# Kernel tuning notes

Measured on AMD Instinct MI355X. Metric: run time of the kernel, lower is better.

Reference implementation:

```python
import jax, jax.numpy as jnp
import numpy as np

N = 100000
E = 1600000
G = 256
D_IN = 128
NEURON = 64
ATT_F = 8
K = 3
ALPHA = 0.1


def setup_inputs() -> dict:
    key = jax.random.key(0)
    ks = jax.random.split(key, 12)
    x = jax.random.normal(ks[0], (N, D_IN), dtype=jnp.float32)
    closeness_feature = jax.random.normal(ks[1], (N, ATT_F), dtype=jnp.float32)
    edge_index = jax.random.randint(ks[2], (2, E), 0, N, dtype=jnp.int32)
    batch = jnp.sort(jax.random.randint(ks[3], (N,), 0, G, dtype=jnp.int32))
    s = 0.05
    return {
        "x": x,
        "closeness_feature": closeness_feature,
        "edge_index": edge_index,
        "batch": batch,
        "num_graphs": G,
        "nn1_w": jax.random.normal(ks[4], (D_IN, NEURON), dtype=jnp.float32) * s,
        "nn1_b": jnp.zeros((NEURON,), dtype=jnp.float32),
        "close_w": jax.random.normal(ks[5], (ATT_F, 1), dtype=jnp.float32) * s,
        "close_b": jnp.zeros((1,), dtype=jnp.float32),
        "att1_w": jax.random.normal(ks[6], (NEURON, 16), dtype=jnp.float32) * s,
        "att1_b": jnp.zeros((16,), dtype=jnp.float32),
        "att2_w": jax.random.normal(ks[7], (16, 1), dtype=jnp.float32) * s,
        "att2_b": jnp.zeros((1,), dtype=jnp.float32),
    }


def _appnp(x, edge_index, n):
    # gcn_norm with self-loops: A_hat = D^{-1/2}(A+I)D^{-1/2}
    loop = jnp.arange(n, dtype=edge_index.dtype)
    src = jnp.concatenate([edge_index[0], loop])
    dst = jnp.concatenate([edge_index[1], loop])
    deg = jax.ops.segment_sum(jnp.ones_like(dst, dtype=x.dtype), dst, num_segments=n)
    dinv = jax.lax.rsqrt(deg)  # deg >= 1 due to self loops
    norm = (dinv[src] * dinv[dst])[:, None]  # [E+N, 1]
    h = x
    for _ in range(K):
        agg = jax.ops.segment_sum(norm * h[src], dst, num_segments=n)
        h = (1.0 - ALPHA) * agg + ALPHA * x
    return h


def reference(x, closeness_feature, edge_index, batch, num_graphs,
              nn1_w, nn1_b, close_w, close_b, att1_w, att1_b, att2_w, att2_b):
    n = x.shape[0]
    h = _appnp(x, edge_index, n)                      # [N, D_IN]
    h = jax.nn.relu(h @ nn1_w + nn1_b)                # [N, 64]

    # per-graph softmax over closeness scores (segment softmax)
    logits = (closeness_feature @ close_w + close_b)[:, 0]          # [N]
    m = jax.ops.segment_max(logits, batch, num_segments=num_graphs)  # [G]
    w = jnp.exp(logits - m[batch])
    z = jax.ops.segment_sum(w, batch, num_segments=num_graphs)       # [G]
    p = w / z[batch]                                                 # softmax per graph

    cnt = jax.ops.segment_sum(jnp.ones((n,), dtype=h.dtype), batch,
                              num_segments=num_graphs)               # nodes per graph
    p = p * cnt[batch]                                               # scaled by curr_size

    # self_max: per-graph max over weighted node features
    pooled = jax.ops.segment_max(p[:, None] * h, batch, num_segments=num_graphs)  # [G, 64]

    a = jax.nn.relu(pooled @ att1_w + att1_b)         # [G, 16]
    return a @ att2_w + att2_b                        # [G, 1]
```

## Files before the change

### kernel.cpp

```cpp
#include <hip/hip_runtime.h>
#include <cstdint>
#include <cstddef>


#define DIN 128
#define NEU 64
#define BK2 512
#define BKSHIFT2 9
#define BKCAP 16384
#define ESCAP 12288
#define MAXNB 256
#define ASTAGE 6400

typedef __attribute__((ext_vector_type(8))) short short8v;
typedef __attribute__((ext_vector_type(4))) float f32x4;

__device__ inline float bf2f(unsigned short h) {
    return __uint_as_float(((unsigned)h) << 16);
}
__device__ inline unsigned short f2bf(float f) {
    unsigned u = __float_as_uint(f);
    unsigned r = u + 0x7FFFu + ((u >> 16) & 1u);
    return (unsigned short)(r >> 16);
}


__global__ __launch_bounds__(256) void binA_kernel(
        const int* __restrict__ src, const int* __restrict__ dst,
        int* __restrict__ bcur, int* __restrict__ pk, int E, int NB) {
    __shared__ int hist[MAXNB];
    __shared__ int lstart[MAXNB];
    __shared__ int lcur[MAXNB];
    __shared__ int resv[MAXNB];
    __shared__ int sh[256];
    __shared__ int stage[ASTAGE];
    __shared__ int gidx[ASTAGE];
    int nchunk = gridDim.x;
    int chunk = (E + nchunk - 1) / nchunk;
    int lo = blockIdx.x * chunk;
    int hi = min(E, lo + chunk);
    int t = threadIdx.x;
    for (int b = t; b < NB; b += 256) hist[b] = 0;
    __syncthreads();
    for (int i = lo + t; i < hi; i += 256)
        atomicAdd(&hist[dst[i] >> BKSHIFT2], 1);
    __syncthreads();
    int c = (t < NB) ? hist[t] : 0;
    sh[t] = c;
    __syncthreads();
    for (int d = 1; d < 256; d <<= 1) {
        int u = (t >= d) ? sh[t - d] : 0;
        __syncthreads();
        sh[t] += u;
        __syncthreads();
    }
    if (t < NB) {
        int excl = sh[t] - c;
        lstart[t] = excl;
        lcur[t] = excl;
        resv[t] = atomicAdd(&bcur[t], c);
    }
    __syncthreads();
    for (int i = lo + t; i < hi; i += 256) {
        int d = dst[i], b = d >> BKSHIFT2;
        int p = atomicAdd(&lcur[b], 1);
        stage[p] = (src[i] << BKSHIFT2) | (d & (BK2 - 1));
        gidx[p] = resv[b] + (p - lstart[b]) + b * BKCAP;
    }
    __syncthreads();
    int total = hi - lo;
    for (int q = t; q < total; q += 256)
        pk[gidx[q]] = stage[q];
}


__global__ __launch_bounds__(256) void binB_kernel(
        const int* __restrict__ bcur, const int* __restrict__ pk,
        int* __restrict__ es, int* __restrict__ rowptr,
        float* __restrict__ dinv, int N, int NB) {
    __shared__ int cur[BK2];
    __shared__ int sh[256];
    __shared__ int esl[ESCAP];
    __shared__ int sbase[2];
    int b = blockIdx.x;
    int t = threadIdx.x;
    int node0 = b << BKSHIFT2;
    int v = (t < NB) ? bcur[t] : 0;
    sh[t] = v;
    __syncthreads();
    for (int d = 1; d < 256; d <<= 1) {
        int u = (t >= d) ? sh[t - d] : 0;
        __syncthreads();
        sh[t] += u;
        __syncthreads();
    }
    if (t == b) { sbase[0] = sh[t] - v; sbase[1] = v; }
    __syncthreads();
    int base = sbase[0];
    int count = sbase[1];
    const int* pb = pk + (size_t)b * BKCAP;

    for (int q = t; q < BK2; q += 256) cur[q] = 0;
    __syncthreads();
    for (int i = t; i < count; i += 256)
        atomicAdd(&cur[pb[i] & (BK2 - 1)], 1);
    __syncthreads();
    int c0 = cur[2 * t], c1 = cur[2 * t + 1];
    int s = c0 + c1;
    __syncthreads();
    sh[t] = s;
    __syncthreads();
    for (int d = 1; d < 256; d <<= 1) {
        int u = (t >= d) ? sh[t - d] : 0;
        __syncthreads();
        sh[t] += u;
        __syncthreads();
    }
    int excl = sh[t] - s;
    int n0 = node0 + 2 * t;
    if (n0 < N) {
        rowptr[n0 + 1] = base + excl + c0;
        dinv[n0] = rsqrtf((float)c0 + 1.0f);
    }
    if (n0 + 1 < N) {
        rowptr[n0 + 2] = base + excl + c0 + c1;
        dinv[n0 + 1] = rsqrtf((float)c1 + 1.0f);
    }
    if (b == 0 && t == 0) rowptr[0] = 0;
    __syncthreads();
    cur[2 * t] = excl;
    cur[2 * t + 1] = excl + c0;
    __syncthreads();
    for (int i = t; i < count; i += 256) {
        int w = pb[i];
        int pos = atomicAdd(&cur[w & (BK2 - 1)], 1);
        if (pos < ESCAP) esl[pos] = w >> BKSHIFT2;
    }
    __syncthreads();
    for (int i = t; i < count; i += 256) es[base + i] = esl[i];
}


__global__ __launch_bounds__(256) void fc1_kernel(
        const float* __restrict__ x, const float* __restrict__ W,
        const float* __restrict__ dinv, ushort* __restrict__ yb,
        ushort* __restrict__ g0, ushort* __restrict__ g1,
        ushort* __restrict__ g2, int N) {
    int tid = threadIdx.x;
    if (blockIdx.x == 0 && tid < 48) {
        int buf = tid >> 4, e = tid & 15;
        ushort* gp = (buf == 0) ? g0 : (buf == 1) ? g1 : g2;
        ((ushort4*)(gp + (size_t)N * NEU))[e] = make_ushort4(0, 0, 0, 0);
    }
    __shared__ ushort sW[DIN * NEU];
    for (int k = tid; k < DIN * NEU / 2; k += 256) {
        float2 v = ((const float2*)W)[k];
        ushort2 o;
        o.x = f2bf(v.x);
        o.y = f2bf(v.y);
        ((ushort2*)sW)[k] = o;
    }
    __syncthreads();
    int lane = tid & 63;
    int wv = tid >> 6;
    int l15 = lane & 15;
    int lg = lane >> 4;
    short8v bfrag[4][4];
#pragma unroll
    for (int kt = 0; kt < 4; kt++)
#pragma unroll
        for (int ct = 0; ct < 4; ct++) {
            short8v f;
#pragma unroll
            for (int e = 0; e < 8; e++)
                f[e] = (short)sW[(kt * 32 + lg * 8 + e) * NEU + ct * 16 + l15];
            bfrag[kt][ct] = f;
        }
    long long row0 = (long long)blockIdx.x * 64 + wv * 16;
    if (row0 >= N) return;
    bool rowok = (row0 + l15) < N;
    const float* xr = x + (size_t)(row0 + l15) * DIN;
    f32x4 acc[4];
#pragma unroll
    for (int ct = 0; ct < 4; ct++) acc[ct] = (f32x4){0.f, 0.f, 0.f, 0.f};
#pragma unroll
    for (int kt = 0; kt < 4; kt++) {
        short8v af = (short8v){0, 0, 0, 0, 0, 0, 0, 0};
        if (rowok) {
            float4 v0 = *((const float4*)(xr + kt * 32 + lg * 8));
            float4 v1 = *((const float4*)(xr + kt * 32 + lg * 8 + 4));
            af[0] = (short)f2bf(v0.x); af[1] = (short)f2bf(v0.y);
            af[2] = (short)f2bf(v0.z); af[3] = (short)f2bf(v0.w);
            af[4] = (short)f2bf(v1.x); af[5] = (short)f2bf(v1.y);
            af[6] = (short)f2bf(v1.z); af[7] = (short)f2bf(v1.w);
        }
#pragma unroll
        for (int ct = 0; ct < 4; ct++)
            acc[ct] = __builtin_amdgcn_mfma_f32_16x16x32_bf16(af, bfrag[kt][ct], acc[ct], 0, 0, 0);
    }
#pragma unroll
    for (int r = 0; r < 4; r++) {
        long long rr = row0 + lg * 4 + r;
        if (rr < N) {
            float dv = dinv[rr];
#pragma unroll
            for (int ct = 0; ct < 4; ct++) {
                float v = acc[ct][r];
                yb[(size_t)rr * NEU + ct * 16 + l15] = f2bf(v);
                g0[(size_t)rr * NEU + ct * 16 + l15] = f2bf(dv * v);
            }
        }
    }
}


__device__ inline void acc4(float4& a, ushort4 w) {
    a.x += bf2f(w.x); a.y += bf2f(w.y); a.z += bf2f(w.z); a.w += bf2f(w.w);
}

template <int MODE>
__global__ __launch_bounds__(256) void pull_kernel(
        const int* __restrict__ rowptr, const int* __restrict__ es,
        const float* __restrict__ dinv, const ushort* __restrict__ gin,
        const ushort* __restrict__ yb, const float* __restrict__ b1,
        ushort* __restrict__ gout, float* __restrict__ h2out, int N) {
    int wid = threadIdx.x >> 6;
    int lane = threadIdx.x & 63;
    int quarter = lane >> 4;
    int l16 = lane & 15;
    int node = blockIdx.x * 4 + wid;
    if (node >= N) return;
    int beg = rowptr[node], end = rowptr[node + 1];
    float dd = dinv[node];
    const ushort4* gin4 = (const ushort4*)gin;
    float4 a0 = make_float4(0.f, 0.f, 0.f, 0.f);
    float4 a1 = make_float4(0.f, 0.f, 0.f, 0.f);
    float4 a2 = make_float4(0.f, 0.f, 0.f, 0.f);
    float4 a3 = make_float4(0.f, 0.f, 0.f, 0.f);
    int deg = end - beg;
    for (int base = 0; base < deg; base += 64) {
        int myi = base + lane;
        int msrc = (myi < deg) ? es[beg + myi] : N;
        int cnt = min(64, deg - base);
        int quads = (cnt + 3) >> 2;
        int j = 0;
        for (; j + 3 < quads; j += 4) {
            int s0 = __shfl(msrc, 4 * j + quarter);
            int s1 = __shfl(msrc, 4 * j + 4 + quarter);
            int s2 = __shfl(msrc, 4 * j + 8 + quarter);
            int s3 = __shfl(msrc, 4 * j + 12 + quarter);
            ushort4 w0 = gin4[(uint)(s0 << 4) + l16];
            ushort4 w1 = gin4[(uint)(s1 << 4) + l16];
            ushort4 w2 = gin4[(uint)(s2 << 4) + l16];
            ushort4 w3 = gin4[(uint)(s3 << 4) + l16];
            acc4(a0, w0); acc4(a1, w1); acc4(a2, w2); acc4(a3, w3);
        }
        for (; j < quads; j++) {
            int s0 = __shfl(msrc, 4 * j + quarter);
            ushort4 w0 = gin4[(uint)(s0 << 4) + l16];
            acc4(a0, w0);
        }
    }
    float4 acc;
    acc.x = (a0.x + a1.x) + (a2.x + a3.x);
    acc.y = (a0.y + a1.y) + (a2.y + a3.y);
    acc.z = (a0.z + a1.z) + (a2.z + a3.z);
    acc.w = (a0.w + a1.w) + (a2.w + a3.w);
    acc.x += __shfl_xor(acc.x, 16);
    acc.y += __shfl_xor(acc.y, 16);
    acc.z += __shfl_xor(acc.z, 16);
    acc.w += __shfl_xor(acc.w, 16);
    acc.x += __shfl_xor(acc.x, 32);
    acc.y += __shfl_xor(acc.y, 32);
    acc.z += __shfl_xor(acc.z, 32);
    acc.w += __shfl_xor(acc.w, 32);
    if (quarter == 0) {
        ushort4 gv = *((const ushort4*)(gin + (size_t)node * NEU) + l16);
        ushort4 yv = *((const ushort4*)(yb + (size_t)node * NEU) + l16);
        float c9 = 0.9f * dd;
        float hx = c9 * (acc.x + bf2f(gv.x)) + 0.1f * bf2f(yv.x);
        float hy = c9 * (acc.y + bf2f(gv.y)) + 0.1f * bf2f(yv.y);
        float hz = c9 * (acc.z + bf2f(gv.z)) + 0.1f * bf2f(yv.z);
        float hw = c9 * (acc.w + bf2f(gv.w)) + 0.1f * bf2f(yv.w);
        if (MODE == 1) {
            float4 bb = *((const float4*)b1 + l16);
            float4 o;
            o.x = fmaxf(hx + bb.x, 0.f);
            o.y = fmaxf(hy + bb.y, 0.f);
            o.z = fmaxf(hz + bb.z, 0.f);
            o.w = fmaxf(hw + bb.w, 0.f);
            *((float4*)(h2out + (size_t)node * NEU) + l16) = o;
        } else {
            ushort4 o;
            o.x = f2bf(dd * hx); o.y = f2bf(dd * hy);
            o.z = f2bf(dd * hz); o.w = f2bf(dd * hw);
            *((ushort4*)(gout + (size_t)node * NEU) + l16) = o;
        }
    }
}


__global__ __launch_bounds__(256) void head_kernel(
        const int* __restrict__ batch, const float* __restrict__ cf,
        const float* __restrict__ cw, const float* __restrict__ cb,
        const float* __restrict__ h2, const float* __restrict__ aw1,
        const float* __restrict__ ab1, const float* __restrict__ aw2,
        const float* __restrict__ ab2, float* __restrict__ out, int N) {
    int g = blockIdx.x;
    int tid = threadIdx.x;
    __shared__ int sbound[2];
    __shared__ float redm[256];
    __shared__ float redz[256];
    __shared__ float pooled[64];
    __shared__ float sa[16];
    if (tid < 2) {
        int target = g + tid;
        int lo = 0, hi = N;
        while (lo < hi) {
            int mid = (lo + hi) >> 1;
            if (batch[mid] < target) lo = mid + 1; else hi = mid;
        }
        sbound[tid] = lo;
    }
    __syncthreads();
    int s0 = sbound[0], e0 = sbound[1];
    float w0 = cw[0], w1 = cw[1], w2 = cw[2], w3 = cw[3];
    float w4 = cw[4], w5 = cw[5], w6 = cw[6], w7 = cw[7];
    float cb0 = cb[0];
    float m = -INFINITY, z = 0.f;
    for (int i = s0 + tid; i < e0; i += 256) {
        const float4* c = (const float4*)(cf + (size_t)i * 8);
        float4 A = c[0], B = c[1];
        float l = A.x * w0 + A.y * w1 + A.z * w2 + A.w * w3
                + B.x * w4 + B.y * w5 + B.z * w6 + B.w * w7 + cb0;
        float mn = fmaxf(m, l);
        z = z * __expf(m - mn) + __expf(l - mn);
        m = mn;
    }
    redm[tid] = m; redz[tid] = z;
    __syncthreads();
    for (int w = 128; w > 0; w >>= 1) {
        if (tid < w) {
            float ma = redm[tid], mb = redm[tid + w];
            float za = redz[tid], zb = redz[tid + w];
            float mn = fmaxf(ma, mb);
            redz[tid] = (mn == -INFINITY) ? 0.f
                       : za * __expf(ma - mn) + zb * __expf(mb - mn);
            redm[tid] = mn;
        }
        __syncthreads();
    }
    float M = redm[0];
    float scale = (float)(e0 - s0) / redz[0];
    __syncthreads();
    int j = tid & 63, r = tid >> 6;
    float mx = -INFINITY;
    for (int i = s0 + r; i < e0; i += 4) {
        const float4* c = (const float4*)(cf + (size_t)i * 8);
        float4 A = c[0], B = c[1];
        float l = A.x * w0 + A.y * w1 + A.z * w2 + A.w * w3
                + B.x * w4 + B.y * w5 + B.z * w6 + B.w * w7 + cb0;
        float p = __expf(l - M) * scale;
        mx = fmaxf(mx, p * h2[(size_t)i * NEU + j]);
    }
    redm[tid] = mx;
    __syncthreads();
    if (r == 0)
        pooled[j] = fmaxf(fmaxf(redm[j], redm[64 + j]),
                          fmaxf(redm[128 + j], redm[192 + j]));
    __syncthreads();
    if (tid < 16) {
        float acc = ab1[tid];
#pragma unroll
        for (int k = 0; k < 64; k++) acc = fmaf(pooled[k], aw1[k * 16 + tid], acc);
        sa[tid] = fmaxf(acc, 0.f);
    }
    __syncthreads();
    if (tid == 0) {
        float o = ab2[0];
#pragma unroll
        for (int k = 0; k < 16; k++) o = fmaf(sa[k], aw2[k], o);
        out[g] = o;
    }
}


extern "C" void kernel_launch(void* const* d_in, const int* in_sizes, int n_in,
                              void* d_out, int out_size, void* d_ws, size_t ws_size,
                              hipStream_t stream) {
    const float* x       = (const float*)d_in[0];
    const float* cf      = (const float*)d_in[1];
    const int*   ei      = (const int*)d_in[2];
    const int*   batch   = (const int*)d_in[3];
    const float* nn1_w   = (const float*)d_in[5];
    const float* nn1_b   = (const float*)d_in[6];
    const float* close_w = (const float*)d_in[7];
    const float* close_b = (const float*)d_in[8];
    const float* att1_w  = (const float*)d_in[9];
    const float* att1_b  = (const float*)d_in[10];
    const float* att2_w  = (const float*)d_in[11];
    const float* att2_b  = (const float*)d_in[12];
    float* out = (float*)d_out;

    int N = in_sizes[0] / DIN;
    int E = in_sizes[2] / 2;
    int G = out_size;

    const int* src = ei;
    const int* dst = ei + E;

    char* w = (char*)d_ws;
    size_t off = 0;
    auto alloc = [&](size_t bytes) -> void* {
        void* ptr = w + off;
        off += (bytes + 511) & ~(size_t)511;
        return ptr;
    };
    int NB = (N + BK2 - 1) >> BKSHIFT2;

    ushort* yb     = (ushort*)alloc((size_t)N * NEU * 2);
    ushort* g0     = (ushort*)alloc(((size_t)N + 1) * NEU * 2);
    ushort* g1     = (ushort*)alloc(((size_t)N + 1) * NEU * 2);
    ushort* g2     = (ushort*)alloc(((size_t)N + 1) * NEU * 2);
    float* h2      = (float*)alloc((size_t)N * NEU * 4);
    float* dinv    = (float*)alloc((size_t)N * 4);
    int*   rowptr  = (int*)alloc(((size_t)N + 1) * 4);
    int*   es      = (int*)alloc((size_t)E * 4);
    int*   bcur    = (int*)alloc((size_t)NB * 4);
    int*   pk      = (int*)alloc((size_t)NB * BKCAP * 4);
    (void)ws_size; (void)n_in;

    hipMemsetAsync(bcur, 0, (size_t)NB * 4, stream);

    binA_kernel<<<256, 256, 0, stream>>>(src, dst, bcur, pk, E, NB);
    binB_kernel<<<NB, 256, 0, stream>>>(bcur, pk, es, rowptr, dinv, N, NB);

    fc1_kernel<<<(N + 63) / 64, 256, 0, stream>>>(x, nn1_w, dinv, yb, g0, g1, g2, N);

    pull_kernel<0><<<(N + 3) / 4, 256, 0, stream>>>(rowptr, es, dinv, g0, yb, nn1_b, g1, nullptr, N);
    pull_kernel<0><<<(N + 3) / 4, 256, 0, stream>>>(rowptr, es, dinv, g1, yb, nn1_b, g2, nullptr, N);
    pull_kernel<1><<<(N + 3) / 4, 256, 0, stream>>>(rowptr, es, dinv, g2, yb, nn1_b, nullptr, h2, N);

    head_kernel<<<G, 256, 0, stream>>>(batch, cf, close_w, close_b, h2,
                                       att1_w, att1_b, att2_w, att2_b, out, N);
}
```

Measured before the change: 238.4 us.

## Fuse edge binning with fc1 GEMM and simplify pull gather loop

Merges the edge-binning pass and the fc1 MFMA GEMM into one launch, with block ranges split by role, so the independent GEMM runs concurrently with binning. The dinv scaling that produces g0 moves into the CSR-build kernel, which reads back yb per bucket. The pull kernel now reads edge indices straight from memory per quarter-wave instead of staging them through shuffles, and drops the padded sentinel rows. This shrinks launch count and lets the edge staging and the GEMM overlap, at the cost of an extra read of yb and less unrolling in the gather loop.

```diff
diff --git a/kernel.cpp b/kernel.cpp
--- a/kernel.cpp
+++ b/kernel.cpp
@@ -10,7 +10,7 @@
 #define BKCAP 16384
 #define ESCAP 12288
 #define MAXNB 256
-#define ASTAGE 6400
+#define ASTAGE 3200
 
 typedef __attribute__((ext_vector_type(8))) short short8v;
 typedef __attribute__((ext_vector_type(4))) float f32x4;
@@ -25,59 +25,118 @@
 }
 
 
-__global__ __launch_bounds__(256) void binA_kernel(
+__global__ __launch_bounds__(256) void binA_fc1_kernel(
         const int* __restrict__ src, const int* __restrict__ dst,
-        int* __restrict__ bcur, int* __restrict__ pk, int E, int NB) {
-    __shared__ int hist[MAXNB];
-    __shared__ int lstart[MAXNB];
-    __shared__ int lcur[MAXNB];
-    __shared__ int resv[MAXNB];
-    __shared__ int sh[256];
-    __shared__ int stage[ASTAGE];
-    __shared__ int gidx[ASTAGE];
-    int nchunk = gridDim.x;
-    int chunk = (E + nchunk - 1) / nchunk;
-    int lo = blockIdx.x * chunk;
-    int hi = min(E, lo + chunk);
+        int* __restrict__ bcur, int* __restrict__ pk, int E, int NB, int nbinA,
+        const float* __restrict__ x, const float* __restrict__ W,
+        ushort* __restrict__ yb, int N) {
+    __shared__ int smem[1280 + 2 * ASTAGE];
     int t = threadIdx.x;
-    for (int b = t; b < NB; b += 256) hist[b] = 0;
-    __syncthreads();
-    for (int i = lo + t; i < hi; i += 256)
-        atomicAdd(&hist[dst[i] >> BKSHIFT2], 1);
-    __syncthreads();
-    int c = (t < NB) ? hist[t] : 0;
-    sh[t] = c;
-    __syncthreads();
-    for (int d = 1; d < 256; d <<= 1) {
-        int u = (t >= d) ? sh[t - d] : 0;
-        __syncthreads();
-        sh[t] += u;
-        __syncthreads();
-    }
-    if (t < NB) {
-        int excl = sh[t] - c;
-        lstart[t] = excl;
-        lcur[t] = excl;
-        resv[t] = atomicAdd(&bcur[t], c);
-    }
-    __syncthreads();
-    for (int i = lo + t; i < hi; i += 256) {
-        int d = dst[i], b = d >> BKSHIFT2;
-        int p = atomicAdd(&lcur[b], 1);
-        stage[p] = (src[i] << BKSHIFT2) | (d & (BK2 - 1));
-        gidx[p] = resv[b] + (p - lstart[b]) + b * BKCAP;
-    }
-    __syncthreads();
-    int total = hi - lo;
-    for (int q = t; q < total; q += 256)
-        pk[gidx[q]] = stage[q];
+    if ((int)blockIdx.x < nbinA) {
+        int* hist   = smem;
+        int* lstart = smem + 256;
+        int* lcur   = smem + 512;
+        int* resv   = smem + 768;
+        int* sh     = smem + 1024;
+        int* stage  = smem + 1280;
+        int* gidx   = smem + 1280 + ASTAGE;
+        int chunk = (E + nbinA - 1) / nbinA;
+        int lo = blockIdx.x * chunk;
+        int hi = min(E, lo + chunk);
+        for (int b = t; b < NB; b += 256) hist[b] = 0;
+        __syncthreads();
+        for (int i = lo + t; i < hi; i += 256)
+            atomicAdd(&hist[dst[i] >> BKSHIFT2], 1);
+        __syncthreads();
+        int c = (t < NB) ? hist[t] : 0;
+        sh[t] = c;
+        __syncthreads();
+        for (int d = 1; d < 256; d <<= 1) {
+            int u = (t >= d) ? sh[t - d] : 0;
+            __syncthreads();
+            sh[t] += u;
+            __syncthreads();
+        }
+        if (t < NB) {
+            int excl = sh[t] - c;
+            lstart[t] = excl;
+            lcur[t] = excl;
+            resv[t] = atomicAdd(&bcur[t], c);
+        }
+        __syncthreads();
+        for (int i = lo + t; i < hi; i += 256) {
+            int d = dst[i], b = d >> BKSHIFT2;
+            int p = atomicAdd(&lcur[b], 1);
+            stage[p] = (src[i] << BKSHIFT2) | (d & (BK2 - 1));
+            gidx[p] = resv[b] + (p - lstart[b]) + b * BKCAP;
+        }
+        __syncthreads();
+        int total = hi - lo;
+        for (int q = t; q < total; q += 256)
+            pk[gidx[q]] = stage[q];
+    } else {
+        ushort* sW = (ushort*)smem;
+        for (int k = t; k < DIN * NEU / 2; k += 256) {
+            float2 v = ((const float2*)W)[k];
+            ushort2 o;
+            o.x = f2bf(v.x);
+            o.y = f2bf(v.y);
+            ((ushort2*)sW)[k] = o;
+        }
+        __syncthreads();
+        int lane = t & 63;
+        int wv = t >> 6;
+        int l15 = lane & 15;
+        int lg = lane >> 4;
+        short8v bfrag[4][4];
+#pragma unroll
+        for (int kt = 0; kt < 4; kt++)
+#pragma unroll
+            for (int ct = 0; ct < 4; ct++) {
+                short8v f;
+#pragma unroll
+                for (int e = 0; e < 8; e++)
+                    f[e] = (short)sW[(kt * 32 + lg * 8 + e) * NEU + ct * 16 + l15];
+                bfrag[kt][ct] = f;
+            }
+        long long row0 = (long long)(blockIdx.x - nbinA) * 64 + wv * 16;
+        if (row0 >= N) return;
+        bool rowok = (row0 + l15) < N;
+        const float* xr = x + (size_t)(row0 + l15) * DIN;
+        f32x4 acc[4];
+#pragma unroll
+        for (int ct = 0; ct < 4; ct++) acc[ct] = (f32x4){0.f, 0.f, 0.f, 0.f};
+#pragma unroll
+        for (int kt = 0; kt < 4; kt++) {
+            short8v af = (short8v){0, 0, 0, 0, 0, 0, 0, 0};
+            if (rowok) {
+                float4 v0 = *((const float4*)(xr + kt * 32 + lg * 8));
+                float4 v1 = *((const float4*)(xr + kt * 32 + lg * 8 + 4));
+                af[0] = (short)f2bf(v0.x); af[1] = (short)f2bf(v0.y);
+                af[2] = (short)f2bf(v0.z); af[3] = (short)f2bf(v0.w);
+                af[4] = (short)f2bf(v1.x); af[5] = (short)f2bf(v1.y);
+                af[6] = (short)f2bf(v1.z); af[7] = (short)f2bf(v1.w);
+            }
+#pragma unroll
+            for (int ct = 0; ct < 4; ct++)
+                acc[ct] = __builtin_amdgcn_mfma_f32_16x16x32_bf16(af, bfrag[kt][ct], acc[ct], 0, 0, 0);
+        }
+#pragma unroll
+        for (int ct = 0; ct < 4; ct++)
+#pragma unroll
+            for (int r = 0; r < 4; r++) {
+                long long rr = row0 + lg * 4 + r;
+                if (rr < N) yb[(size_t)rr * NEU + ct * 16 + l15] = f2bf(acc[ct][r]);
+            }
+    }
 }
 
 
 __global__ __launch_bounds__(256) void binB_kernel(
         const int* __restrict__ bcur, const int* __restrict__ pk,
         int* __restrict__ es, int* __restrict__ rowptr,
-        float* __restrict__ dinv, int N, int NB) {
+        float* __restrict__ dinv, const ushort* __restrict__ yb,
+        ushort* __restrict__ g0, int N, int NB) {
     __shared__ int cur[BK2];
     __shared__ int sh[256];
     __shared__ int esl[ESCAP];
@@ -107,6 +166,8 @@
     __syncthreads();
     int c0 = cur[2 * t], c1 = cur[2 * t + 1];
     int s = c0 + c1;
+    float dv0 = rsqrtf((float)c0 + 1.0f);
+    float dv1 = rsqrtf((float)c1 + 1.0f);
     __syncthreads();
     sh[t] = s;
     __syncthreads();
@@ -120,11 +181,11 @@
     int n0 = node0 + 2 * t;
     if (n0 < N) {
         rowptr[n0 + 1] = base + excl + c0;
-        dinv[n0] = rsqrtf((float)c0 + 1.0f);
+        dinv[n0] = dv0;
     }
     if (n0 + 1 < N) {
         rowptr[n0 + 2] = base + excl + c0 + c1;
-        dinv[n0 + 1] = rsqrtf((float)c1 + 1.0f);
+        dinv[n0 + 1] = dv1;
     }
     if (b == 0 && t == 0) rowptr[0] = 0;
     __syncthreads();
@@ -138,77 +199,23 @@
     }
     __syncthreads();
     for (int i = t; i < count; i += 256) es[base + i] = esl[i];
-}
-
-
-__global__ __launch_bounds__(256) void fc1_kernel(
-        const float* __restrict__ x, const float* __restrict__ W,
-        const float* __restrict__ dinv, ushort* __restrict__ yb,
-        ushort* __restrict__ g0, ushort* __restrict__ g1,
-        ushort* __restrict__ g2, int N) {
-    int tid = threadIdx.x;
-    if (blockIdx.x == 0 && tid < 48) {
-        int buf = tid >> 4, e = tid & 15;
-        ushort* gp = (buf == 0) ? g0 : (buf == 1) ? g1 : g2;
-        ((ushort4*)(gp + (size_t)N * NEU))[e] = make_ushort4(0, 0, 0, 0);
-    }
-    __shared__ ushort sW[DIN * NEU];
-    for (int k = tid; k < DIN * NEU / 2; k += 256) {
-        float2 v = ((const float2*)W)[k];
-        ushort2 o;
-        o.x = f2bf(v.x);
-        o.y = f2bf(v.y);
-        ((ushort2*)sW)[k] = o;
-    }
-    __syncthreads();
-    int lane = tid & 63;
-    int wv = tid >> 6;
-    int l15 = lane & 15;
-    int lg = lane >> 4;
-    short8v bfrag[4][4];
-#pragma unroll
-    for (int kt = 0; kt < 4; kt++)
-#pragma unroll
-        for (int ct = 0; ct < 4; ct++) {
-            short8v f;
-#pragma unroll
-            for (int e = 0; e < 8; e++)
-                f[e] = (short)sW[(kt * 32 + lg * 8 + e) * NEU + ct * 16 + l15];
-            bfrag[kt][ct] = f;
-        }
-    long long row0 = (long long)blockIdx.x * 64 + wv * 16;
-    if (row0 >= N) return;
-    bool rowok = (row0 + l15) < N;
-    const float* xr = x + (size_t)(row0 + l15) * DIN;
-    f32x4 acc[4];
-#pragma unroll
-    for (int ct = 0; ct < 4; ct++) acc[ct] = (f32x4){0.f, 0.f, 0.f, 0.f};
-#pragma unroll
-    for (int kt = 0; kt < 4; kt++) {
-        short8v af = (short8v){0, 0, 0, 0, 0, 0, 0, 0};
-        if (rowok) {
-            float4 v0 = *((const float4*)(xr + kt * 32 + lg * 8));
-            float4 v1 = *((const float4*)(xr + kt * 32 + lg * 8 + 4));
-            af[0] = (short)f2bf(v0.x); af[1] = (short)f2bf(v0.y);
-            af[2] = (short)f2bf(v0.z); af[3] = (short)f2bf(v0.w);
-            af[4] = (short)f2bf(v1.x); af[5] = (short)f2bf(v1.y);
-            af[6] = (short)f2bf(v1.z); af[7] = (short)f2bf(v1.w);
-        }
-#pragma unroll
-        for (int ct = 0; ct < 4; ct++)
-            acc[ct] = __builtin_amdgcn_mfma_f32_16x16x32_bf16(af, bfrag[kt][ct], acc[ct], 0, 0, 0);
-    }
-#pragma unroll
-    for (int r = 0; r < 4; r++) {
-        long long rr = row0 + lg * 4 + r;
-        if (rr < N) {
-            float dv = dinv[rr];
-#pragma unroll
-            for (int ct = 0; ct < 4; ct++) {
-                float v = acc[ct][r];
-                yb[(size_t)rr * NEU + ct * 16 + l15] = f2bf(v);
-                g0[(size_t)rr * NEU + ct * 16 + l15] = f2bf(dv * v);
-            }
+    __syncthreads();
+    float* fdinv = (float*)cur;
+    fdinv[2 * t] = dv0;
+    fdinv[2 * t + 1] = dv1;
+    __syncthreads();
+    for (int q = t; q < BK2 * 16; q += 256) {
+        int ln = q >> 4, el = q & 15;
+        int n = node0 + ln;
+        if (n < N) {
+            float dv = fdinv[ln];
+            ushort4 w = *((const ushort4*)(yb + (size_t)n * NEU) + el);
+            ushort4 o;
+            o.x = f2bf(dv * bf2f(w.x));
+            o.y = f2bf(dv * bf2f(w.y));
+            o.z = f2bf(dv * bf2f(w.z));
+            o.w = f2bf(dv * bf2f(w.w));
+            *((ushort4*)(g0 + (size_t)n * NEU) + el) = o;
         }
     }
 }
@@ -235,37 +242,25 @@
     const ushort4* gin4 = (const ushort4*)gin;
     float4 a0 = make_float4(0.f, 0.f, 0.f, 0.f);
     float4 a1 = make_float4(0.f, 0.f, 0.f, 0.f);
-    float4 a2 = make_float4(0.f, 0.f, 0.f, 0.f);
-    float4 a3 = make_float4(0.f, 0.f, 0.f, 0.f);
-    int deg = end - beg;
-    for (int base = 0; base < deg; base += 64) {
-        int myi = base + lane;
-        int msrc = (myi < deg) ? es[beg + myi] : N;
-        int cnt = min(64, deg - base);
-        int quads = (cnt + 3) >> 2;
-        int j = 0;
-        for (; j + 3 < quads; j += 4) {
-            int s0 = __shfl(msrc, 4 * j + quarter);
-            int s1 = __shfl(msrc, 4 * j + 4 + quarter);
-            int s2 = __shfl(msrc, 4 * j + 8 + quarter);
-            int s3 = __shfl(msrc, 4 * j + 12 + quarter);
-            ushort4 w0 = gin4[(uint)(s0 << 4) + l16];
-            ushort4 w1 = gin4[(uint)(s1 << 4) + l16];
-            ushort4 w2 = gin4[(uint)(s2 << 4) + l16];
-            ushort4 w3 = gin4[(uint)(s3 << 4) + l16];
-            acc4(a0, w0); acc4(a1, w1); acc4(a2, w2); acc4(a3, w3);
-        }
-        for (; j < quads; j++) {
-            int s0 = __shfl(msrc, 4 * j + quarter);
-            ushort4 w0 = gin4[(uint)(s0 << 4) + l16];
-            acc4(a0, w0);
-        }
+    int e = beg + quarter;
+    for (; e + 4 < end; e += 8) {
+        int s0 = es[e];
+        int s1 = es[e + 4];
+        ushort4 w0 = gin4[(uint)(s0 << 4) + l16];
+        ushort4 w1 = gin4[(uint)(s1 << 4) + l16];
+        acc4(a0, w0);
+        acc4(a1, w1);
+    }
+    if (e < end) {
+        int s0 = es[e];
+        ushort4 w0 = gin4[(uint)(s0 << 4) + l16];
+        acc4(a0, w0);
     }
     float4 acc;
-    acc.x = (a0.x + a1.x) + (a2.x + a3.x);
-    acc.y = (a0.y + a1.y) + (a2.y + a3.y);
-    acc.z = (a0.z + a1.z) + (a2.z + a3.z);
-    acc.w = (a0.w + a1.w) + (a2.w + a3.w);
+    acc.x = a0.x + a1.x;
+    acc.y = a0.y + a1.y;
+    acc.z = a0.z + a1.z;
+    acc.w = a0.w + a1.w;
     acc.x += __shfl_xor(acc.x, 16);
     acc.y += __shfl_xor(acc.y, 16);
     acc.z += __shfl_xor(acc.z, 16);
@@ -417,11 +412,13 @@
         return ptr;
     };
     int NB = (N + BK2 - 1) >> BKSHIFT2;
+    int nbinA = (E + ASTAGE - 1) / ASTAGE;
+    int fc1b = (N + 63) / 64;
 
     ushort* yb     = (ushort*)alloc((size_t)N * NEU * 2);
-    ushort* g0     = (ushort*)alloc(((size_t)N + 1) * NEU * 2);
-    ushort* g1     = (ushort*)alloc(((size_t)N + 1) * NEU * 2);
-    ushort* g2     = (ushort*)alloc(((size_t)N + 1) * NEU * 2);
+    ushort* g0     = (ushort*)alloc((size_t)N * NEU * 2);
+    ushort* g1     = (ushort*)alloc((size_t)N * NEU * 2);
+    ushort* g2     = (ushort*)alloc((size_t)N * NEU * 2);
     float* h2      = (float*)alloc((size_t)N * NEU * 4);
     float* dinv    = (float*)alloc((size_t)N * 4);
     int*   rowptr  = (int*)alloc(((size_t)N + 1) * 4);
@@ -432,10 +429,10 @@
 
     hipMemsetAsync(bcur, 0, (size_t)NB * 4, stream);
 
-    binA_kernel<<<256, 256, 0, stream>>>(src, dst, bcur, pk, E, NB);
-    binB_kernel<<<NB, 256, 0, stream>>>(bcur, pk, es, rowptr, dinv, N, NB);
-
-    fc1_kernel<<<(N + 63) / 64, 256, 0, stream>>>(x, nn1_w, dinv, yb, g0, g1, g2, N);
+    binA_fc1_kernel<<<nbinA + fc1b, 256, 0, stream>>>(
+        src, dst, bcur, pk, E, NB, nbinA, x, nn1_w, yb, N);
+
+    binB_kernel<<<NB, 256, 0, stream>>>(bcur, pk, es, rowptr, dinv, yb, g0, N, NB);
 
     pull_kernel<0><<<(N + 3) / 4, 256, 0, stream>>>(rowptr, es, dinv, g0, yb, nn1_b, g1, nullptr, N);
     pull_kernel<0><<<(N + 3) / 4, 256, 0, stream>>>(rowptr, es, dinv, g1, yb, nn1_b, g2, nullptr, N);
```

New measurement: 263.3 us. +10.4%, slower.

## Halve bucket size and fold dinv-scaled g0 production into binB

Applied to the files above, without the earlier changes.

Buckets shrink from 512 to 256 nodes, so binB launches about 391 blocks instead of 196 and each block needs less shared memory. That gives more parallelism and occupancy. fc1 now runs first and writes only yb, and binB computes g0 = dinv*yb for its own nodes, which removes fc1's dependency on dinv. The bucket-base prefix scan becomes a per-block reduction. In exchange yb is read back once more, and the per-bucket caps (ESCAP 8192) must still hold the edge counts per bucket, roughly 4096 on average.

```diff
diff --git a/kernel.cpp b/kernel.cpp
--- a/kernel.cpp
+++ b/kernel.cpp
@@ -5,11 +5,11 @@
 
 #define DIN 128
 #define NEU 64
-#define BK2 512
-#define BKSHIFT2 9
-#define BKCAP 16384
-#define ESCAP 12288
-#define MAXNB 256
+#define BK2 256
+#define BKSHIFT2 8
+#define BKCAP 8192
+#define ESCAP 8192
+#define MAXNB 512
 #define ASTAGE 6400
 
 typedef __attribute__((ext_vector_type(8))) short short8v;
@@ -40,13 +40,14 @@
     int lo = blockIdx.x * chunk;
     int hi = min(E, lo + chunk);
     int t = threadIdx.x;
-    for (int b = t; b < NB; b += 256) hist[b] = 0;
+    for (int b = t; b < MAXNB; b += 256) hist[b] = 0;
     __syncthreads();
     for (int i = lo + t; i < hi; i += 256)
         atomicAdd(&hist[dst[i] >> BKSHIFT2], 1);
     __syncthreads();
-    int c = (t < NB) ? hist[t] : 0;
-    sh[t] = c;
+    int c0 = hist[2 * t], c1 = hist[2 * t + 1];
+    int s = c0 + c1;
+    sh[t] = s;
     __syncthreads();
     for (int d = 1; d < 256; d <<= 1) {
         int u = (t >= d) ? sh[t - d] : 0;
@@ -54,12 +55,11 @@
         sh[t] += u;
         __syncthreads();
     }
-    if (t < NB) {
-        int excl = sh[t] - c;
-        lstart[t] = excl;
-        lcur[t] = excl;
-        resv[t] = atomicAdd(&bcur[t], c);
-    }
+    int excl = sh[t] - s;
+    lstart[2 * t] = excl;       lcur[2 * t] = excl;
+    lstart[2 * t + 1] = excl + c0; lcur[2 * t + 1] = excl + c0;
+    resv[2 * t]     = (c0 > 0) ? atomicAdd(&bcur[2 * t], c0) : 0;
+    resv[2 * t + 1] = (c1 > 0) ? atomicAdd(&bcur[2 * t + 1], c1) : 0;
     __syncthreads();
     for (int i = lo + t; i < hi; i += 256) {
         int d = dst[i], b = d >> BKSHIFT2;
@@ -77,7 +77,9 @@
 __global__ __launch_bounds__(256) void binB_kernel(
         const int* __restrict__ bcur, const int* __restrict__ pk,
         int* __restrict__ es, int* __restrict__ rowptr,
-        float* __restrict__ dinv, int N, int NB) {
+        float* __restrict__ dinv, const ushort* __restrict__ yb,
+        ushort* __restrict__ g0, ushort* __restrict__ g1,
+        ushort* __restrict__ g2, int N, int NB) {
     __shared__ int cur[BK2];
     __shared__ int sh[256];
     __shared__ int esl[ESCAP];
@@ -85,30 +87,34 @@
     int b = blockIdx.x;
     int t = threadIdx.x;
     int node0 = b << BKSHIFT2;
-    int v = (t < NB) ? bcur[t] : 0;
-    sh[t] = v;
-    __syncthreads();
-    for (int d = 1; d < 256; d <<= 1) {
-        int u = (t >= d) ? sh[t - d] : 0;
-        __syncthreads();
-        sh[t] += u;
-        __syncthreads();
-    }
-    if (t == b) { sbase[0] = sh[t] - v; sbase[1] = v; }
+    if (b == 0 && t < 24) {
+        int buf = t >> 3, e = t & 7;
+        ushort* gp = (buf == 0) ? g0 : (buf == 1) ? g1 : g2;
+        ((uint4*)(gp + (size_t)N * NEU))[e] = make_uint4(0, 0, 0, 0);
+    }
+    int partial = 0;
+    if (t < b) partial += bcur[t];
+    if (t + 256 < b) partial += bcur[t + 256];
+    sh[t] = partial;
+    __syncthreads();
+    for (int w = 128; w > 0; w >>= 1) {
+        if (t < w) sh[t] += sh[t + w];
+        __syncthreads();
+    }
+    if (t == 0) { sbase[0] = sh[0]; sbase[1] = bcur[b]; }
     __syncthreads();
     int base = sbase[0];
     int count = sbase[1];
     const int* pb = pk + (size_t)b * BKCAP;
 
-    for (int q = t; q < BK2; q += 256) cur[q] = 0;
+    cur[t] = 0;
     __syncthreads();
     for (int i = t; i < count; i += 256)
         atomicAdd(&cur[pb[i] & (BK2 - 1)], 1);
     __syncthreads();
-    int c0 = cur[2 * t], c1 = cur[2 * t + 1];
-    int s = c0 + c1;
-    __syncthreads();
-    sh[t] = s;
+    int c = cur[t];
+    float dv = rsqrtf((float)c + 1.0f);
+    sh[t] = c;
     __syncthreads();
     for (int d = 1; d < 256; d <<= 1) {
         int u = (t >= d) ? sh[t - d] : 0;
@@ -116,20 +122,16 @@
         sh[t] += u;
         __syncthreads();
     }
-    int excl = sh[t] - s;
-    int n0 = node0 + 2 * t;
+    int incl = sh[t];
+    int excl = incl - c;
+    int n0 = node0 + t;
     if (n0 < N) {
-        rowptr[n0 + 1] = base + excl + c0;
-        dinv[n0] = rsqrtf((float)c0 + 1.0f);
-    }
-    if (n0 + 1 < N) {
-        rowptr[n0 + 2] = base + excl + c0 + c1;
-        dinv[n0 + 1] = rsqrtf((float)c1 + 1.0f);
+        rowptr[n0 + 1] = base + incl;
+        dinv[n0] = dv;
     }
     if (b == 0 && t == 0) rowptr[0] = 0;
     __syncthreads();
-    cur[2 * t] = excl;
-    cur[2 * t + 1] = excl + c0;
+    cur[t] = excl;
     __syncthreads();
     for (int i = t; i < count; i += 256) {
         int w = pb[i];
@@ -138,21 +140,32 @@
     }
     __syncthreads();
     for (int i = t; i < count; i += 256) es[base + i] = esl[i];
+    __syncthreads();
+    float* fdinv = (float*)sh;
+    fdinv[t] = dv;
+    __syncthreads();
+    for (int q = t; q < BK2 * 16; q += 256) {
+        int ln = q >> 4, el = q & 15;
+        int n = node0 + ln;
+        if (n < N) {
+            float d2 = fdinv[ln];
+            ushort4 w = *((const ushort4*)(yb + (size_t)n * NEU) + el);
+            ushort4 o;
+            o.x = f2bf(d2 * bf2f(w.x));
+            o.y = f2bf(d2 * bf2f(w.y));
+            o.z = f2bf(d2 * bf2f(w.z));
+            o.w = f2bf(d2 * bf2f(w.w));
+            *((ushort4*)(g0 + (size_t)n * NEU) + el) = o;
+        }
+    }
 }
 
 
 __global__ __launch_bounds__(256) void fc1_kernel(
         const float* __restrict__ x, const float* __restrict__ W,
-        const float* __restrict__ dinv, ushort* __restrict__ yb,
-        ushort* __restrict__ g0, ushort* __restrict__ g1,
-        ushort* __restrict__ g2, int N) {
+        ushort* __restrict__ yb, int N) {
+    __shared__ ushort sW[DIN * NEU];
     int tid = threadIdx.x;
-    if (blockIdx.x == 0 && tid < 48) {
-        int buf = tid >> 4, e = tid & 15;
-        ushort* gp = (buf == 0) ? g0 : (buf == 1) ? g1 : g2;
-        ((ushort4*)(gp + (size_t)N * NEU))[e] = make_ushort4(0, 0, 0, 0);
-    }
-    __shared__ ushort sW[DIN * NEU];
     for (int k = tid; k < DIN * NEU / 2; k += 256) {
         float2 v = ((const float2*)W)[k];
         ushort2 o;
@@ -199,18 +212,12 @@
             acc[ct] = __builtin_amdgcn_mfma_f32_16x16x32_bf16(af, bfrag[kt][ct], acc[ct], 0, 0, 0);
     }
 #pragma unroll
-    for (int r = 0; r < 4; r++) {
-        long long rr = row0 + lg * 4 + r;
-        if (rr < N) {
-            float dv = dinv[rr];
-#pragma unroll
-            for (int ct = 0; ct < 4; ct++) {
-                float v = acc[ct][r];
-                yb[(size_t)rr * NEU + ct * 16 + l15] = f2bf(v);
-                g0[(size_t)rr * NEU + ct * 16 + l15] = f2bf(dv * v);
-            }
-        }
-    }
+    for (int ct = 0; ct < 4; ct++)
+#pragma unroll
+        for (int r = 0; r < 4; r++) {
+            long long rr = row0 + lg * 4 + r;
+            if (rr < N) yb[(size_t)rr * NEU + ct * 16 + l15] = f2bf(acc[ct][r]);
+        }
 }
 
 
@@ -426,16 +433,17 @@
     float* dinv    = (float*)alloc((size_t)N * 4);
     int*   rowptr  = (int*)alloc(((size_t)N + 1) * 4);
     int*   es      = (int*)alloc((size_t)E * 4);
-    int*   bcur    = (int*)alloc((size_t)NB * 4);
-    int*   pk      = (int*)alloc((size_t)NB * BKCAP * 4);
+    int*   bcur    = (int*)alloc((size_t)MAXNB * 4);
+    int*   pk      = (int*)alloc((size_t)MAXNB * BKCAP * 4);
     (void)ws_size; (void)n_in;
 
-    hipMemsetAsync(bcur, 0, (size_t)NB * 4, stream);
+    hipMemsetAsync(bcur, 0, (size_t)MAXNB * 4, stream);
+
+    fc1_kernel<<<(N + 63) / 64, 256, 0, stream>>>(x, nn1_w, yb, N);
 
     binA_kernel<<<256, 256, 0, stream>>>(src, dst, bcur, pk, E, NB);
-    binB_kernel<<<NB, 256, 0, stream>>>(bcur, pk, es, rowptr, dinv, N, NB);
-
-    fc1_kernel<<<(N + 63) / 64, 256, 0, stream>>>(x, nn1_w, dinv, yb, g0, g1, g2, N);
+    binB_kernel<<<NB, 256, 0, stream>>>(bcur, pk, es, rowptr, dinv, yb,
+                                        g0, g1, g2, N, NB);
 
     pull_kernel<0><<<(N + 3) / 4, 256, 0, stream>>>(rowptr, es, dinv, g0, yb, nn1_b, g1, nullptr, N);
     pull_kernel<0><<<(N + 3) / 4, 256, 0, stream>>>(rowptr, es, dinv, g1, yb, nn1_b, g2, nullptr, N);
```

Measured after the change: 242.4 us. Within noise of the previous version (+1.6%).
